# Performance work log

Measured on AMD Instinct MI355X. Metric: run time of the kernel, lower is better.

Reference implementation:

```python
import jax, jax.numpy as jnp
import numpy as np

EPS = 1e-6        # RMSNorm140 eps
LAM = 0.1         # lambda_: second-order score weight
HAD = 0.05        # hadamard_scale

def _rmsnorm(x, w):
    return x * jax.lax.rsqrt(jnp.mean(x * x, axis=-1, keepdims=True) + EPS) * w

def _rope(x):
    # x: [b, h, s, d]; interleaved-pair rotary embedding (theta=10000)
    b, h, s, d = x.shape
    inv = 1.0 / (10000.0 ** (jnp.arange(0, d, 2, dtype=jnp.float32) / d))
    ang = jnp.arange(s, dtype=jnp.float32)[:, None] * inv[None, :]  # [s, d/2]
    cos, sin = jnp.cos(ang), jnp.sin(ang)
    x1, x2 = x[..., 0::2], x[..., 1::2]
    out = jnp.stack([x1 * cos - x2 * sin, x1 * sin + x2 * cos], axis=-1)
    return out.reshape(b, h, s, d)

def _rotate_half(x):
    d = x.shape[-1] // 2
    return jnp.concatenate([-x[..., d:], x[..., :d]], axis=-1)

def _attn_pass(Q, K, V):
    # scores = (Q@K^T + lam * Q^2 @ (K^2)^T) / sqrt(head_dim)   (second-order amplify)
    scale = 1.0 / jnp.sqrt(jnp.float32(Q.shape[-1]))
    scores = (jnp.einsum('bhsd,bhtd->bhst', Q, K)
              + LAM * jnp.einsum('bhsd,bhtd->bhst', Q * Q, K * K)) * scale
    return jnp.einsum('bhst,bhtd->bhsd', jax.nn.softmax(scores, axis=-1), V)

def _attention(x, wq, wk, wv, wo, gate_w):
    b, s, dim = x.shape
    hd = gate_w.shape[0]
    nh = dim // hd
    def proj(w):  # StickyLinear: x @ W^T, W stored [out, in]
        return (x @ w.T).reshape(b, s, nh, hd).transpose(0, 2, 1, 3)  # [b,h,s,d]
    Q, K, V = proj(wq), proj(wk), proj(wv)
    Q, K = _rope(Q), _rope(K)
    out1 = _attn_pass(Q, K, V)
    # rotated second pass + per-channel sigmoid gate over head_dim
    out2 = _attn_pass(_rotate_half(Q), _rotate_half(K), V)
    g = jax.nn.sigmoid(gate_w)
    out = out1 * (1.0 - g) + out2 * g
    out = out + HAD * out * out  # Hadamard mix (elementwise nonlinearity)
    out = out.transpose(0, 2, 1, 3).reshape(b, s, dim)
    return out @ wo.T

def _ffn(x, w1, w3, w2):
    # SwiGLU: down( silu(gate(x)) * up(x) )
    return (jax.nn.silu(x @ w1.T) * (x @ w3.T)) @ w2.T

def reference(x, norm1_w, norm2_w, wq, wk, wv, wo, gate_w, w1, w3, w2):
    h = x + _attention(_rmsnorm(x, norm1_w), wq, wk, wv, wo, gate_w)
    return h + _ffn(_rmsnorm(h, norm2_w), w1, w3, w2)

def setup_inputs() -> dict:
    B, S, D, NH, DFF = 2, 1024, 2048, 16, 8192
    HD = D // NH
    key = jax.random.key(0)
    ks = jax.random.split(key, 9)
    std = 0.02
    return {
        'x': jax.random.normal(ks[0], (B, S, D), dtype=jnp.float32),
        'norm1_w': jnp.ones((D,), jnp.float32),
        'norm2_w': jnp.ones((D,), jnp.float32),
        'wq': jax.random.normal(ks[1], (D, D), jnp.float32) * std,
        'wk': jax.random.normal(ks[2], (D, D), jnp.float32) * std,
        'wv': jax.random.normal(ks[3], (D, D), jnp.float32) * std,
        'wo': jax.random.normal(ks[4], (D, D), jnp.float32) * std,
        'gate_w': jax.random.normal(ks[5], (HD,), jnp.float32) * 0.01,
        'w1': jax.random.normal(ks[6], (DFF, D), jnp.float32) * std,
        'w3': jax.random.normal(ks[7], (DFF, D), jnp.float32) * std,
        'w2': jax.random.normal(ks[8], (D, DFF), jnp.float32) * std,
    }
```

## Files before the change

### kernel.cpp

```cpp
#include <hip/hip_runtime.h>
#include <hip/hip_bf16.h>

typedef unsigned short u16;
typedef unsigned int u32;
typedef u16 u16x8 __attribute__((ext_vector_type(8)));
typedef float f32x4 __attribute__((ext_vector_type(4)));

__device__ __forceinline__ u16 f2bf(float f) {
  union { float f; u32 u; } v; v.f = f;
  u32 r = v.u + 0x7FFFu + ((v.u >> 16) & 1u);
  return (u16)(r >> 16);
}
__device__ __forceinline__ float bf2f(u16 h) {
  union { u32 u; float f; } v; v.u = ((u32)h) << 16;
  return v.f;
}
__device__ __forceinline__ void mfma_bf16_16x16x32(f32x4& acc, const f32x4& a, const f32x4& b) {
  asm("v_mfma_f32_16x16x32_bf16 %0, %1, %2, %0" : "+v"(acc) : "v"(a), "v"(b));
}
__device__ __forceinline__ void gload_lds16(const void* g, void* l) {
  __builtin_amdgcn_global_load_lds(
      (const __attribute__((address_space(1))) unsigned int*)g,
      (__attribute__((address_space(3))) unsigned int*)l, 16, 0, 0);
}

__global__ __launch_bounds__(256) void cvt_k(const float* __restrict__ src,
                                             u16* __restrict__ dst, int n8) {
  int i = blockIdx.x * 256 + threadIdx.x;
  if (i >= n8) return;
  float4 f0 = *(const float4*)&src[(size_t)i * 8];
  float4 f1 = *(const float4*)&src[(size_t)i * 8 + 4];
  u16x8 o;
  o[0] = f2bf(f0.x); o[1] = f2bf(f0.y); o[2] = f2bf(f0.z); o[3] = f2bf(f0.w);
  o[4] = f2bf(f1.x); o[5] = f2bf(f1.y); o[6] = f2bf(f1.z); o[7] = f2bf(f1.w);
  *(u16x8*)&dst[(size_t)i * 8] = o;
}

__global__ __launch_bounds__(256) void cvt13_k(const float* __restrict__ src,
                                               u16* __restrict__ dst, int half) {
  int r = blockIdx.x;
  int dr = ((r >> 4) << 5) + (r & 15) + (half << 4);
  int t = threadIdx.x;
  const float* s = src + (size_t)r * 2048 + t * 8;
  float4 f0 = *(const float4*)s;
  float4 f1 = *(const float4*)(s + 4);
  u16x8 o;
  o[0] = f2bf(f0.x); o[1] = f2bf(f0.y); o[2] = f2bf(f0.z); o[3] = f2bf(f0.w);
  o[4] = f2bf(f1.x); o[5] = f2bf(f1.y); o[6] = f2bf(f1.z); o[7] = f2bf(f1.w);
  *(u16x8*)&dst[(size_t)dr * 2048 + t * 8] = o;
}

__global__ __launch_bounds__(256) void rmsnorm_k(const float* __restrict__ X,
                                                 const float* __restrict__ W,
                                                 u16* __restrict__ O) {
  const int row = blockIdx.x;
  const int tid = threadIdx.x;
  const float* x = X + (size_t)row * 2048;
  float4 v0 = *(const float4*)&x[tid * 8];
  float4 v1 = *(const float4*)&x[tid * 8 + 4];
  float s = v0.x * v0.x + v0.y * v0.y + v0.z * v0.z + v0.w * v0.w
          + v1.x * v1.x + v1.y * v1.y + v1.z * v1.z + v1.w * v1.w;
  #pragma unroll
  for (int m = 1; m < 64; m <<= 1) s += __shfl_xor(s, m);
  __shared__ float red[4];
  if ((tid & 63) == 0) red[tid >> 6] = s;
  __syncthreads();
  float tot = red[0] + red[1] + red[2] + red[3];
  float r = rsqrtf(tot * (1.0f / 2048.0f) + 1e-6f);
  float4 w0 = *(const float4*)&W[tid * 8];
  float4 w1 = *(const float4*)&W[tid * 8 + 4];
  u16x8 o;
  o[0] = f2bf(v0.x * r * w0.x); o[1] = f2bf(v0.y * r * w0.y);
  o[2] = f2bf(v0.z * r * w0.z); o[3] = f2bf(v0.w * r * w0.w);
  o[4] = f2bf(v1.x * r * w1.x); o[5] = f2bf(v1.y * r * w1.y);
  o[6] = f2bf(v1.z * r * w1.z); o[7] = f2bf(v1.w * r * w1.w);
  *(u16x8*)&O[(size_t)row * 2048 + tid * 8] = o;
}

#define EPI_F32 0
#define EPI_ADDF32 1
#define EPI_SWIGLU 2

template <int EPI>
__global__ __launch_bounds__(256) void gemm_bt(const u16* __restrict__ A,
                                               const u16* __restrict__ B,
                                               float* __restrict__ Cf,
                                               u16* __restrict__ Cb,
                                               const float* __restrict__ R,
                                               int M, int N, int Kt,
                                               int lda, int ldb) {
  __shared__ __align__(16) u16 As[2][128 * 32];
  __shared__ __align__(16) u16 Bs[2][128 * 32];
  const int tid = threadIdx.x;
  const int lane = tid & 63;
  const int w = tid >> 6;
  const int wm = w >> 1, wn = w & 1;
  const int m0 = blockIdx.y * 128, n0 = blockIdx.x * 128;
  const int z = blockIdx.z;
  A += (size_t)z * Kt;
  B += (size_t)z * Kt;
  Cf += (size_t)z * M * N;
  const int r0 = tid >> 2;
  const int c0 = (tid & 3) * 8;
  const int r1 = r0 + 64;
  const int laneM = lane & 15;
  const int laneK = (lane >> 4) * 8;

  f32x4 acc[4][4];
  #pragma unroll
  for (int i = 0; i < 4; i++)
    #pragma unroll
    for (int j = 0; j < 4; j++) acc[i][j] = (f32x4){0.f, 0.f, 0.f, 0.f};

  const u16* Ar0 = &A[(size_t)(m0 + r0) * lda + c0];
  const u16* Ar1 = &A[(size_t)(m0 + r1) * lda + c0];
  const u16* Br0 = &B[(size_t)(n0 + r0) * ldb + c0];
  const u16* Br1 = &B[(size_t)(n0 + r1) * ldb + c0];
  const int lofs0 = r0 * 32 + c0;
  const int lofs1 = r1 * 32 + c0;

  auto stage = [&](int bsel, int kt) {
    gload_lds16(Ar0 + kt, &As[bsel][lofs0]);
    gload_lds16(Ar1 + kt, &As[bsel][lofs1]);
    gload_lds16(Br0 + kt, &Bs[bsel][lofs0]);
    gload_lds16(Br1 + kt, &Bs[bsel][lofs1]);
  };

  stage(0, 0);
  const int nt = Kt >> 5;
  for (int t = 0; t < nt; t++) {
    const int cur = t & 1;
    if (t + 1 < nt) {
      stage(cur ^ 1, (t + 1) << 5);
      asm volatile("s_waitcnt vmcnt(4)" ::: "memory");
    } else {
      asm volatile("s_waitcnt vmcnt(0)" ::: "memory");
    }
    __builtin_amdgcn_s_barrier();
    f32x4 af[4], bfr[4];
    #pragma unroll
    for (int mi = 0; mi < 4; mi++)
      af[mi] = *(const f32x4*)&As[cur][(wm * 64 + mi * 16 + laneM) * 32 + laneK];
    #pragma unroll
    for (int ni = 0; ni < 4; ni++)
      bfr[ni] = *(const f32x4*)&Bs[cur][(wn * 64 + ni * 16 + laneM) * 32 + laneK];
    #pragma unroll
    for (int mi = 0; mi < 4; mi++)
      #pragma unroll
      for (int ni = 0; ni < 4; ni++)
        mfma_bf16_16x16x32(acc[mi][ni], af[mi], bfr[ni]);
    __builtin_amdgcn_s_barrier();
  }

  const int rowb = (lane >> 4) * 4;
  const int coll = lane & 15;
  #pragma unroll
  for (int mi = 0; mi < 4; mi++) {
    #pragma unroll
    for (int i = 0; i < 4; i++) {
      int row = m0 + wm * 64 + mi * 16 + rowb + i;
      #pragma unroll
      for (int ni = 0; ni < 4; ni++) {
        int col = n0 + wn * 64 + ni * 16 + coll;
        size_t idx = (size_t)row * N + col;
        float v = acc[mi][ni][i];
        if constexpr (EPI == EPI_F32) Cf[idx] = v;
        else Cf[idx] = v + R[idx];
      }
    }
  }
}

template <int EPI>
__global__ __launch_bounds__(512, 2) void gemm256(const u16* __restrict__ A,
                                                  const u16* __restrict__ B,
                                                  float* __restrict__ Cf,
                                                  u16* __restrict__ Cb,
                                                  int M, int N, int Kt,
                                                  int lda, int ldb) {
  __shared__ __align__(16) char sm[131072];
  const int tid = threadIdx.x;
  const int lane = tid & 63, w = tid >> 6;
  const int wr = w >> 2, wc = w & 3;
  const int laneM = lane & 15, laneG = lane >> 4;
  const int m0 = blockIdx.y * 256, n0 = blockIdx.x * 256;
  const int z = blockIdx.z;
  A += (size_t)z * Kt;
  B += (size_t)z * Kt;
  Cf += (size_t)z * M * N;

  const int srow = tid >> 3;
  const int scb = (tid & 7) * 16;

  f32x4 acc[8][4];
  #pragma unroll
  for (int i = 0; i < 8; i++)
    #pragma unroll
    for (int j = 0; j < 4; j++) acc[i][j] = (f32x4){0.f, 0.f, 0.f, 0.f};

  auto stage = [&](int buf, int ktE, int ht) {
    const int half = ht & 1;
    const bool isA = ht < 2;
    char* base = sm + (isA ? 0 : 65536) + buf * 32768 + half * 16384;
    const u16* src = isA ? A : B;
    const int ld = isA ? lda : ldb;
    const int rb = (isA ? m0 : n0) + half * 128;
    #pragma unroll
    for (int j = 0; j < 2; j++) {
      int row = j * 64 + srow;
      int scol = (scb ^ ((row & 7) << 4)) >> 1;
      gload_lds16(src + (size_t)(rb + row) * ld + ktE + scol,
                  base + j * 8192 + tid * 16);
    }
  };

  const int nkt = Kt >> 6;
  #pragma unroll
  for (int ht = 0; ht < 4; ht++) stage(0, 0, ht);

  const int bHalf = wc >> 1;
  const int bRow0 = (wc & 1) * 64;

  for (int t = 0; t < nkt; t++) {
    const int cb_ = t & 1;
    char* aBase = sm + cb_ * 32768 + wr * 16384;
    char* bBase = sm + 65536 + cb_ * 32768 + bHalf * 16384;
    const bool pre = (t + 1 < nkt);
    const int ktE1 = (t + 1) << 6;

    if (pre) {
      #pragma unroll
      for (int ht = 0; ht < 4; ht++) stage(cb_ ^ 1, ktE1, ht);
      asm volatile("s_waitcnt vmcnt(8)" ::: "memory");
    } else {
      asm volatile("s_waitcnt vmcnt(0)" ::: "memory");
    }
    __builtin_amdgcn_s_barrier();

    f32x4 af0[4][2], af1[4][2], bg[4][2];
    #pragma unroll
    for (int ni = 0; ni < 4; ni++)
      #pragma unroll
      for (int ks = 0; ks < 2; ks++) {
        int r = bRow0 + ni * 16 + laneM;
        int cbv = ks * 64 + laneG * 16;
        bg[ni][ks] = *(const f32x4*)(bBase + r * 128 + (cbv ^ ((r & 7) << 4)));
      }
    #pragma unroll
    for (int mi = 0; mi < 4; mi++)
      #pragma unroll
      for (int ks = 0; ks < 2; ks++) {
        int r = mi * 16 + laneM;
        int cbv = ks * 64 + laneG * 16;
        af0[mi][ks] = *(const f32x4*)(aBase + r * 128 + (cbv ^ ((r & 7) << 4)));
      }
    #pragma unroll
    for (int mi = 0; mi < 4; mi++)
      #pragma unroll
      for (int ks = 0; ks < 2; ks++) {
        int r = (4 + mi) * 16 + laneM;
        int cbv = ks * 64 + laneG * 16;
        af1[mi][ks] = *(const f32x4*)(aBase + r * 128 + (cbv ^ ((r & 7) << 4)));
      }

    __builtin_amdgcn_s_setprio(1);
    #pragma unroll
    for (int mi = 0; mi < 4; mi++)
      #pragma unroll
      for (int ni = 0; ni < 4; ni++)
        #pragma unroll
        for (int ks = 0; ks < 2; ks++)
          mfma_bf16_16x16x32(acc[mi][ni], af0[mi][ks], bg[ni][ks]);
    #pragma unroll
    for (int mi = 0; mi < 4; mi++)
      #pragma unroll
      for (int ni = 0; ni < 4; ni++)
        #pragma unroll
        for (int ks = 0; ks < 2; ks++)
          mfma_bf16_16x16x32(acc[4 + mi][ni], af1[mi][ks], bg[ni][ks]);
    __builtin_amdgcn_s_setprio(0);
    __builtin_amdgcn_s_barrier();
  }

  #pragma unroll
  for (int mi = 0; mi < 8; mi++) {
    #pragma unroll
    for (int i = 0; i < 4; i++) {
      int row = m0 + wr * 128 + mi * 16 + laneG * 4 + i;
      if constexpr (EPI == EPI_SWIGLU) {
        #pragma unroll
        for (int np = 0; np < 2; np++) {
          float g = acc[mi][np * 2][i];
          float u = acc[mi][np * 2 + 1][i];
          float sg = g / (1.0f + __expf(-g));
          int j = (n0 >> 1) + wc * 32 + np * 16 + laneM;
          Cb[(size_t)row * (N >> 1) + j] = f2bf(sg * u);
        }
      } else {
        #pragma unroll
        for (int ni = 0; ni < 4; ni++) {
          int col = n0 + wc * 64 + ni * 16 + laneM;
          Cf[(size_t)row * N + col] = acc[mi][ni][i];
        }
      }
    }
  }
}

__global__ __launch_bounds__(256) void reduce5_k(const float* __restrict__ P,
                                                 const float* __restrict__ H,
                                                 float* __restrict__ out) {
  size_t i = ((size_t)blockIdx.x * 256 + threadIdx.x) * 4;
  const size_t MN = 4194304;
  float4 a = *(const float4*)&P[i];
  float4 b = *(const float4*)&P[MN + i];
  float4 c = *(const float4*)&P[2 * MN + i];
  float4 d = *(const float4*)&P[3 * MN + i];
  float4 h = *(const float4*)&H[i];
  float4 o;
  o.x = a.x + b.x + c.x + d.x + h.x;
  o.y = a.y + b.y + c.y + d.y + h.y;
  o.z = a.z + b.z + c.z + d.z + h.z;
  o.w = a.w + b.w + c.w + d.w + h.w;
  *(float4*)&out[i] = o;
}

__device__ __forceinline__ void rope_row(const float* __restrict__ src,
                                         u16* __restrict__ dst, int s, int q4) {
  float vv[32];
  #pragma unroll
  for (int t = 0; t < 8; t++) {
    float4 f = *(const float4*)&src[t * 4];
    vv[t * 4] = f.x; vv[t * 4 + 1] = f.y; vv[t * 4 + 2] = f.z; vv[t * 4 + 3] = f.w;
  }
  u16 o1[32], o2[32];
  #pragma unroll
  for (int jl = 0; jl < 16; jl++) {
    int j = q4 * 16 + jl;
    float inv = exp2f(-(float)j * 0.20762050593046014f);
    float ang = (float)s * inv;
    float sn, cs;
    __sincosf(ang, &sn, &cs);
    float a = vv[2 * jl], b = vv[2 * jl + 1];
    float r1 = a * cs - b * sn;
    float r2 = a * sn + b * cs;
    o1[2 * jl] = f2bf(r1);
    o1[2 * jl + 1] = f2bf(r2);
    o2[2 * jl] = f2bf(0.31622776601683794f * r1 * r1);
    o2[2 * jl + 1] = f2bf(0.31622776601683794f * r2 * r2);
  }
  #pragma unroll
  for (int t = 0; t < 4; t++) {
    *(u16x8*)&dst[q4 * 32 + t * 8] = *(const u16x8*)&o1[t * 8];
    *(u16x8*)&dst[128 + q4 * 32 + t * 8] = *(const u16x8*)&o2[t * 8];
  }
}

__global__ __launch_bounds__(256) void qkv_post_k(const float* __restrict__ QKVF,
                                                  u16* __restrict__ Qe,
                                                  u16* __restrict__ Ke,
                                                  u16* __restrict__ Vt) {
  const int st = blockIdx.x;
  const int bh = blockIdx.y;
  const int b = bh >> 4, h = bh & 15;
  const int tid = threadIdx.x;
  {
    int r = tid >> 2, q4 = tid & 3;
    int s = st * 64 + r;
    size_t rowin = ((size_t)b * 1024 + s) * 6144 + h * 128 + q4 * 32;
    size_t rowe = ((size_t)bh * 1024 + s) * 256;
    rope_row(QKVF + rowin, Qe + rowe, s, q4);
    rope_row(QKVF + rowin + 2048, Ke + rowe, s, q4);
  }
  __shared__ __align__(16) u16 vts[128 * 72];
  {
    int r = tid >> 2, q4 = tid & 3;
    int s = st * 64 + r;
    const float* src = QKVF + ((size_t)b * 1024 + s) * 6144 + 4096 + h * 128 + q4 * 32;
    #pragma unroll
    for (int k = 0; k < 32; k += 4) {
      float4 f = *(const float4*)&src[k];
      int d = q4 * 32 + k;
      vts[(d + 0) * 72 + r] = f2bf(f.x);
      vts[(d + 1) * 72 + r] = f2bf(f.y);
      vts[(d + 2) * 72 + r] = f2bf(f.z);
      vts[(d + 3) * 72 + r] = f2bf(f.w);
    }
  }
  __syncthreads();
  {
    int d = tid >> 1, sp = (tid & 1) * 32;
    u16* dst = Vt + ((size_t)bh * 128 + d) * 1024 + st * 64 + sp;
    #pragma unroll
    for (int k = 0; k < 32; k += 8)
      *(u16x8*)&dst[k] = *(const u16x8*)&vts[d * 72 + sp + k];
  }
}

__global__ __launch_bounds__(256, 2) void attn_k(const u16* __restrict__ Qe,
                                                 const u16* __restrict__ Ke,
                                                 const u16* __restrict__ Vt,
                                                 u16* __restrict__ AO) {
  const int bh = blockIdx.x;
  const int qt = blockIdx.y;
  const int b = bh >> 4, h = bh & 15;
  const int tid = threadIdx.x;
  const int w = tid >> 6, lane = tid & 63;
  const int laneM = lane & 15, laneG = lane >> 4;

  __shared__ __align__(16) char smem[57344];
  u16* plu = (u16*)(smem + 49152 + w * 2048);

  const char* KeB = (const char*)Ke + (size_t)bh * 524288;
  const char* VtB = (const char*)Vt + (size_t)bh * 262144;

  const size_t qbase = ((size_t)bh * 1024 + qt * 64 + w * 16 + laneM) * 256 + laneG * 8;
  f32x4 qf[8];
  #pragma unroll
  for (int kk = 0; kk < 8; kk++) qf[kk] = *(const f32x4*)&Qe[qbase + kk * 32];

  float m_i[4], l_i[4];
  #pragma unroll
  for (int i = 0; i < 4; i++) { m_i[i] = -1e30f; l_i[i] = 0.f; }
  f32x4 accO[8];
  #pragma unroll
  for (int n = 0; n < 8; n++) accO[n] = (f32x4){0.f, 0.f, 0.f, 0.f};

  u16x8 kreg[4], vreg[2];
  auto loadRegs = [&](int ktn) {
    const char* ks = KeB + (size_t)ktn * 16384;
    #pragma unroll
    for (int j = 0; j < 4; j++) {
      int p = j * 4096 + tid * 16;
      kreg[j] = *(const u16x8*)(ks + p);
    }
    const char* vs = VtB + (size_t)ktn * 64;
    #pragma unroll
    for (int j = 0; j < 2; j++) {
      int p = j * 4096 + tid * 16;
      int r = p >> 6, x = p & 63;
      vreg[j] = *(const u16x8*)(vs + (size_t)r * 2048 + x);
    }
  };
  auto writeLDS = [&](int bsel) {
    char* kd = smem + (bsel ? 16384 : 0);
    #pragma unroll
    for (int j = 0; j < 4; j++) {
      int p = j * 4096 + tid * 16;
      int r = p >> 9, x = p & 511;
      *(u16x8*)(kd + r * 512 + (x ^ ((r & 7) << 4))) = kreg[j];
    }
    char* vd = smem + 32768 + (bsel ? 8192 : 0);
    #pragma unroll
    for (int j = 0; j < 2; j++) {
      int p = j * 4096 + tid * 16;
      int r = p >> 6, x = p & 63;
      *(u16x8*)(vd + r * 64 + (x ^ (((r >> 1) & 3) << 4))) = vreg[j];
    }
  };

  loadRegs(0);
  writeLDS(0);
  int cur = 0;
  const float scale = 0.08838834764831845f;

  for (int kt = 0; kt < 32; kt++) {
    if (kt < 31) loadRegs(kt + 1);
    __syncthreads();
    const char* Kc = smem + (cur ? 16384 : 0);
    const char* Vc = smem + 32768 + (cur ? 8192 : 0);

    f32x4 accS[2];
    #pragma unroll
    for (int n = 0; n < 2; n++) accS[n] = (f32x4){0.f, 0.f, 0.f, 0.f};
    #pragma unroll
    for (int n = 0; n < 2; n++) {
      int r = n * 16 + laneM;
      const char* krow = Kc + r * 512;
      int sw = (r & 7) << 4;
      #pragma unroll
      for (int kk = 0; kk < 8; kk++) {
        f32x4 kf = *(const f32x4*)(krow + ((kk * 64 + laneG * 16) ^ sw));
        mfma_bf16_16x16x32(accS[n], qf[kk], kf);
      }
    }

    float p[2][4], sf[4];
    #pragma unroll
    for (int i = 0; i < 4; i++) {
      float mx = fmaxf(accS[0][i], accS[1][i]) * scale;
      #pragma unroll
      for (int m = 1; m < 16; m <<= 1) mx = fmaxf(mx, __shfl_xor(mx, m));
      float mnew = fmaxf(m_i[i], mx);
      sf[i] = __expf(m_i[i] - mnew);
      m_i[i] = mnew;
      float p0 = __expf(accS[0][i] * scale - mnew);
      float p1 = __expf(accS[1][i] * scale - mnew);
      p[0][i] = p0; p[1][i] = p1;
      float rs = p0 + p1;
      #pragma unroll
      for (int m = 1; m < 16; m <<= 1) rs += __shfl_xor(rs, m);
      l_i[i] = l_i[i] * sf[i] + rs;
    }
    #pragma unroll
    for (int n = 0; n < 8; n++) {
      accO[n][0] *= sf[0]; accO[n][1] *= sf[1];
      accO[n][2] *= sf[2]; accO[n][3] *= sf[3];
    }

    #pragma unroll
    for (int n = 0; n < 2; n++)
      #pragma unroll
      for (int i = 0; i < 4; i++) {
        int row = laneG * 4 + i;
        int col = n * 16 + laneM;
        plu[row * 64 + (col ^ (((row >> 2) & 3) << 4))] = f2bf(p[n][i]);
      }
    f32x4 pa = *(const f32x4*)&plu[laneM * 64 +
                                   ((laneG * 8) ^ (((laneM >> 2) & 3) << 4))];

    #pragma unroll
    for (int n = 0; n < 8; n++) {
      int r = n * 16 + laneM;
      f32x4 vf = *(const f32x4*)(Vc + r * 64 + ((laneG * 16) ^ (((r >> 1) & 3) << 4)));
      mfma_bf16_16x16x32(accO[n], pa, vf);
    }

    if (kt < 31) writeLDS(cur ^ 1);
    cur ^= 1;
  }

  #pragma unroll
  for (int i = 0; i < 4; i++) {
    float inv_l = 1.f / l_i[i];
    int row = b * 1024 + qt * 64 + w * 16 + laneG * 4 + i;
    #pragma unroll
    for (int n = 0; n < 8; n++) {
      float o = accO[n][i] * inv_l;
      o = o + 0.05f * o * o;
      AO[(size_t)row * 2048 + h * 128 + n * 16 + laneM] = f2bf(o);
    }
  }
}

extern "C" void kernel_launch(void* const* d_in, const int* in_sizes, int n_in,
                              void* d_out, int out_size, void* d_ws, size_t ws_size,
                              hipStream_t stream) {
  const float* x   = (const float*)d_in[0];
  const float* n1w = (const float*)d_in[1];
  const float* n2w = (const float*)d_in[2];
  const float* wq  = (const float*)d_in[3];
  const float* wk  = (const float*)d_in[4];
  const float* wv  = (const float*)d_in[5];
  const float* wo  = (const float*)d_in[6];
  const float* w1  = (const float*)d_in[8];
  const float* w3  = (const float*)d_in[9];
  const float* w2  = (const float*)d_in[10];

  char* ws = (char*)d_ws;
  u16* WQKVb = (u16*)(ws + 0);
  u16* WOb   = (u16*)(ws + 25165824);
  u16* W13b  = (u16*)(ws + 33554432);
  u16* W2b   = (u16*)(ws + 100663296);
  u16* XN    = (u16*)(ws + 134217728);
  float* QKVF = (float*)(ws + 142606336);
  u16* U     = (u16*)(ws + 142606336);
  float* P   = (float*)(ws + 176160768);
  u16* QE    = (u16*)(ws + 192937984);
  u16* KE    = (u16*)(ws + 209715200);
  u16* VT    = (u16*)(ws + 226492416);
  u16* AO    = (u16*)(ws + 234881024);
  float* H   = (float*)(ws + 243269632);

  cvt_k<<<2048, 256, 0, stream>>>(wq, WQKVb, 524288);
  cvt_k<<<2048, 256, 0, stream>>>(wk, WQKVb + 4194304, 524288);
  cvt_k<<<2048, 256, 0, stream>>>(wv, WQKVb + 8388608, 524288);
  cvt_k<<<2048, 256, 0, stream>>>(wo, WOb, 524288);
  cvt13_k<<<8192, 256, 0, stream>>>(w1, W13b, 0);
  cvt13_k<<<8192, 256, 0, stream>>>(w3, W13b, 1);
  cvt_k<<<8192, 256, 0, stream>>>(w2, W2b, 2097152);

  rmsnorm_k<<<2048, 256, 0, stream>>>(x, n1w, XN);

  gemm256<EPI_F32><<<dim3(24, 8), 512, 0, stream>>>(
      XN, WQKVb, QKVF, nullptr, 2048, 6144, 2048, 2048, 2048);

  qkv_post_k<<<dim3(16, 32), 256, 0, stream>>>(QKVF, QE, KE, VT);

  attn_k<<<dim3(32, 16), 256, 0, stream>>>(QE, KE, VT, AO);

  gemm_bt<EPI_ADDF32><<<dim3(16, 16), 256, 0, stream>>>(
      AO, WOb, H, nullptr, x, 2048, 2048, 2048, 2048, 2048);

  rmsnorm_k<<<2048, 256, 0, stream>>>(H, n2w, XN);

  gemm256<EPI_SWIGLU><<<dim3(64, 8), 512, 0, stream>>>(
      XN, W13b, nullptr, U, 2048, 16384, 2048, 2048, 2048);

  gemm256<EPI_F32><<<dim3(8, 8, 4), 512, 0, stream>>>(
      U, W2b, P, nullptr, 2048, 2048, 2048, 8192, 8192);

  reduce5_k<<<4096, 256, 0, stream>>>(P, H, (float*)d_out);
}
```

Baseline: 505.8 us.

## Emit QKV projection as bf16 and reorder gemm256 fragment loads to cut registers

The QKV GEMM now writes bf16 output instead of fp32, and qkv_post_k reads bf16 for the RoPE and V transpose. This halves the intermediate write and read traffic (about 25MB each way) and adds an extra bf16 rounding before RoPE. The gemm256 inner loop also reuses one A-fragment register set, loading the second half after the first MFMA batch, to lower register pressure. This may reduce overlap between LDS reads and MFMAs.

```diff
diff --git a/kernel.cpp b/kernel.cpp
--- a/kernel.cpp
+++ b/kernel.cpp
@@ -80,6 +80,7 @@
 #define EPI_F32 0
 #define EPI_ADDF32 1
 #define EPI_SWIGLU 2
+#define EPI_BF16G 3
 
 template <int EPI>
 __global__ __launch_bounds__(256) void gemm_bt(const u16* __restrict__ A,
@@ -236,8 +237,9 @@
       asm volatile("s_waitcnt vmcnt(0)" ::: "memory");
     }
     __builtin_amdgcn_s_barrier();
-
-    f32x4 af0[4][2], af1[4][2], bg[4][2];
+    __builtin_amdgcn_s_setprio(1);
+
+    f32x4 af[4][2], bg[4][2];
     #pragma unroll
     for (int ni = 0; ni < 4; ni++)
       #pragma unroll
@@ -252,32 +254,31 @@
       for (int ks = 0; ks < 2; ks++) {
         int r = mi * 16 + laneM;
         int cbv = ks * 64 + laneG * 16;
-        af0[mi][ks] = *(const f32x4*)(aBase + r * 128 + (cbv ^ ((r & 7) << 4)));
+        af[mi][ks] = *(const f32x4*)(aBase + r * 128 + (cbv ^ ((r & 7) << 4)));
       }
+    #pragma unroll
+    for (int mi = 0; mi < 4; mi++)
+      #pragma unroll
+      for (int ni = 0; ni < 4; ni++)
+        #pragma unroll
+        for (int ks = 0; ks < 2; ks++)
+          mfma_bf16_16x16x32(acc[mi][ni], af[mi][ks], bg[ni][ks]);
     #pragma unroll
     for (int mi = 0; mi < 4; mi++)
       #pragma unroll
       for (int ks = 0; ks < 2; ks++) {
         int r = (4 + mi) * 16 + laneM;
         int cbv = ks * 64 + laneG * 16;
-        af1[mi][ks] = *(const f32x4*)(aBase + r * 128 + (cbv ^ ((r & 7) << 4)));
+        af[mi][ks] = *(const f32x4*)(aBase + r * 128 + (cbv ^ ((r & 7) << 4)));
       }
-
-    __builtin_amdgcn_s_setprio(1);
     #pragma unroll
     for (int mi = 0; mi < 4; mi++)
       #pragma unroll
       for (int ni = 0; ni < 4; ni++)
         #pragma unroll
         for (int ks = 0; ks < 2; ks++)
-          mfma_bf16_16x16x32(acc[mi][ni], af0[mi][ks], bg[ni][ks]);
-    #pragma unroll
-    for (int mi = 0; mi < 4; mi++)
-      #pragma unroll
-      for (int ni = 0; ni < 4; ni++)
-        #pragma unroll
-        for (int ks = 0; ks < 2; ks++)
-          mfma_bf16_16x16x32(acc[4 + mi][ni], af1[mi][ks], bg[ni][ks]);
+          mfma_bf16_16x16x32(acc[4 + mi][ni], af[mi][ks], bg[ni][ks]);
+
     __builtin_amdgcn_s_setprio(0);
     __builtin_amdgcn_s_barrier();
   }
@@ -295,6 +296,12 @@
           float sg = g / (1.0f + __expf(-g));
           int j = (n0 >> 1) + wc * 32 + np * 16 + laneM;
           Cb[(size_t)row * (N >> 1) + j] = f2bf(sg * u);
+        }
+      } else if constexpr (EPI == EPI_BF16G) {
+        #pragma unroll
+        for (int ni = 0; ni < 4; ni++) {
+          int col = n0 + wc * 64 + ni * 16 + laneM;
+          Cb[(size_t)row * N + col] = f2bf(acc[mi][ni][i]);
         }
       } else {
         #pragma unroll
@@ -325,13 +332,14 @@
   *(float4*)&out[i] = o;
 }
 
-__device__ __forceinline__ void rope_row(const float* __restrict__ src,
+__device__ __forceinline__ void rope_row(const u16* __restrict__ src,
                                          u16* __restrict__ dst, int s, int q4) {
   float vv[32];
   #pragma unroll
-  for (int t = 0; t < 8; t++) {
-    float4 f = *(const float4*)&src[t * 4];
-    vv[t * 4] = f.x; vv[t * 4 + 1] = f.y; vv[t * 4 + 2] = f.z; vv[t * 4 + 3] = f.w;
+  for (int t = 0; t < 4; t++) {
+    u16x8 v = *(const u16x8*)&src[t * 8];
+    #pragma unroll
+    for (int j = 0; j < 8; j++) vv[t * 8 + j] = bf2f(v[j]);
   }
   u16 o1[32], o2[32];
   #pragma unroll
@@ -356,7 +364,7 @@
   }
 }
 
-__global__ __launch_bounds__(256) void qkv_post_k(const float* __restrict__ QKVF,
+__global__ __launch_bounds__(256) void qkv_post_k(const u16* __restrict__ QKVB,
                                                   u16* __restrict__ Qe,
                                                   u16* __restrict__ Ke,
                                                   u16* __restrict__ Vt) {
@@ -369,22 +377,20 @@
     int s = st * 64 + r;
     size_t rowin = ((size_t)b * 1024 + s) * 6144 + h * 128 + q4 * 32;
     size_t rowe = ((size_t)bh * 1024 + s) * 256;
-    rope_row(QKVF + rowin, Qe + rowe, s, q4);
-    rope_row(QKVF + rowin + 2048, Ke + rowe, s, q4);
+    rope_row(QKVB + rowin, Qe + rowe, s, q4);
+    rope_row(QKVB + rowin + 2048, Ke + rowe, s, q4);
   }
   __shared__ __align__(16) u16 vts[128 * 72];
   {
     int r = tid >> 2, q4 = tid & 3;
     int s = st * 64 + r;
-    const float* src = QKVF + ((size_t)b * 1024 + s) * 6144 + 4096 + h * 128 + q4 * 32;
-    #pragma unroll
-    for (int k = 0; k < 32; k += 4) {
-      float4 f = *(const float4*)&src[k];
+    const u16* src = QKVB + ((size_t)b * 1024 + s) * 6144 + 4096 + h * 128 + q4 * 32;
+    #pragma unroll
+    for (int k = 0; k < 32; k += 8) {
+      u16x8 v = *(const u16x8*)&src[k];
       int d = q4 * 32 + k;
-      vts[(d + 0) * 72 + r] = f2bf(f.x);
-      vts[(d + 1) * 72 + r] = f2bf(f.y);
-      vts[(d + 2) * 72 + r] = f2bf(f.z);
-      vts[(d + 3) * 72 + r] = f2bf(f.w);
+      #pragma unroll
+      for (int j = 0; j < 8; j++) vts[(d + j) * 72 + r] = v[j];
     }
   }
   __syncthreads();
@@ -563,7 +569,7 @@
   u16* W13b  = (u16*)(ws + 33554432);
   u16* W2b   = (u16*)(ws + 100663296);
   u16* XN    = (u16*)(ws + 134217728);
-  float* QKVF = (float*)(ws + 142606336);
+  u16* QKVB  = (u16*)(ws + 142606336);
   u16* U     = (u16*)(ws + 142606336);
   float* P   = (float*)(ws + 176160768);
   u16* QE    = (u16*)(ws + 192937984);
@@ -582,10 +588,10 @@
 
   rmsnorm_k<<<2048, 256, 0, stream>>>(x, n1w, XN);
 
-  gemm256<EPI_F32><<<dim3(24, 8), 512, 0, stream>>>(
-      XN, WQKVb, QKVF, nullptr, 2048, 6144, 2048, 2048, 2048);
-
-  qkv_post_k<<<dim3(16, 32), 256, 0, stream>>>(QKVF, QE, KE, VT);
+  gemm256<EPI_BF16G><<<dim3(24, 8), 512, 0, stream>>>(
+      XN, WQKVb, nullptr, QKVB, 2048, 6144, 2048, 2048, 2048);
+
+  qkv_post_k<<<dim3(16, 32), 256, 0, stream>>>(QKVB, QE, KE, VT);
 
   attn_k<<<dim3(32, 16), 256, 0, stream>>>(QE, KE, VT, AO);
 
```

Result: no change. 499.1 us (-1.3%).
